# Kernel tuning notes

Hardware: AMD Instinct MI355X
Metric: run time of the kernel (lower is better)

## Reference

```python
import jax, jax.numpy as jnp
import numpy as np

BETA = 0.25
N_E = 8192
E_DIM = 256


def setup_inputs() -> dict:
    key = jax.random.key(0)
    k1, k2 = jax.random.split(key)
    z = jax.random.normal(k1, (16, E_DIM, 32, 32), dtype=jnp.float32)
    # matches torch init: uniform_(-1/n_e, 1/n_e)
    codebook = jax.random.uniform(k2, (N_E, E_DIM), dtype=jnp.float32,
                                  minval=-1.0 / N_E, maxval=1.0 / N_E)
    return {"z": z, "codebook": codebook}


def reference(z, codebook):
    B, C, H, W = z.shape  # C == e_dim
    zp = jnp.transpose(z, (0, 2, 3, 1))          # [B, H, W, C]
    zf = zp.reshape(-1, C)                       # [N, C], N = B*H*W
    # squared L2 distances: ||z||^2 + ||e||^2 - 2 z.e
    d = (jnp.sum(zf * zf, axis=1, keepdims=True)
         + jnp.sum(codebook * codebook, axis=1)
         - 2.0 * jnp.einsum('nc,kc->nk', zf, codebook))  # [N, n_e]
    min_encoding_indices = jnp.argmin(d, axis=1)         # [N]
    z_q = codebook[min_encoding_indices].reshape(zp.shape)  # [B, H, W, C]
    sg = jax.lax.stop_gradient
    loss = jnp.mean((sg(z_q) - zp) ** 2) + BETA * jnp.mean((z_q - sg(zp)) ** 2)
    # straight-through estimator
    z_q_st = zp + sg(z_q - zp)
    z_q_out = jnp.transpose(z_q_st, (0, 3, 1, 2))  # back to NCHW
    return z_q_out, loss, min_encoding_indices
```

## Files before the change

kernel.cpp:

```cpp
#include <hip/hip_runtime.h>

typedef short s8v __attribute__((ext_vector_type(8)));
typedef float f4v __attribute__((ext_vector_type(4)));
typedef float f4 __attribute__((ext_vector_type(4)));
typedef unsigned short u16v4 __attribute__((ext_vector_type(4)));

#define N_PIX 16384
#define NE    8192
#define EDIM  256
#define ZQ_ELEMS 4194304
#define MARGIN 4.5e-4f
#define NGRP 512

__device__ __forceinline__ float bf2f(unsigned short u) {
    union { unsigned int i; float f; } c; c.i = ((unsigned int)u) << 16; return c.f;
}
__device__ __forceinline__ unsigned short f2bf(float f) {
    unsigned int u = __float_as_uint(f);
    u = (u + 0x7fffu + ((u >> 16) & 1u)) >> 16;
    return (unsigned short)u;
}
__device__ __forceinline__ unsigned short f2bf_down(float f) {
    unsigned int u = __float_as_uint(f);
    unsigned short b = (unsigned short)(u >> 16);
    if ((u & 0xFFFFu) && (u >> 31)) b += 1;
    return b;
}

__device__ __forceinline__ float np_pw128sq(const float* a) {
    float r[8];
    #pragma unroll
    for (int j = 0; j < 8; ++j) r[j] = __fmul_rn(a[j], a[j]);
    for (int i = 8; i < 128; i += 8)
        #pragma unroll
        for (int j = 0; j < 8; ++j) r[j] = __fadd_rn(r[j], __fmul_rn(a[i + j], a[i + j]));
    return __fadd_rn(__fadd_rn(__fadd_rn(r[0], r[1]), __fadd_rn(r[2], r[3])),
                     __fadd_rn(__fadd_rn(r[4], r[5]), __fadd_rn(r[6], r[7])));
}


__global__ __launch_bounds__(256) void vq_pre(const float* __restrict__ z,
                                              const float* __restrict__ cb,
                                              unsigned short* __restrict__ z16,
                                              unsigned short* __restrict__ cb16,
                                              float* __restrict__ esum32,
                                              int do_z) {
    __shared__ unsigned short zl[64 * 66];
    int t = threadIdx.x;
    int bx = blockIdx.x;
    if (bx < 1024) {
        if (!do_z) return;
        int p0 = (bx >> 2) * 64;
        int c0 = (bx & 3) * 64;
        int b = p0 >> 10, hw0 = p0 & 1023;
        const float* src = z + (((size_t)b * 256 + c0) << 10) + hw0;
        #pragma unroll
        for (int i = 0; i < 4; ++i) {
            int idx = i * 256 + t;
            int ch = idx >> 4, pq = idx & 15;
            f4 v = *(const f4*)(src + ((size_t)ch << 10) + pq * 4);
            #pragma unroll
            for (int e = 0; e < 4; ++e) zl[(pq * 4 + e) * 66 + ch] = f2bf(v[e]);
        }
        __syncthreads();
        #pragma unroll
        for (int i = 0; i < 2; ++i) {
            int idx = i * 256 + t;
            int px = idx >> 3, cc = idx & 7;
            s8v o;
            #pragma unroll
            for (int e = 0; e < 8; ++e) o[e] = (short)zl[px * 66 + cc * 8 + e];
            *(s8v*)&z16[((size_t)(p0 + px)) * 256 + c0 + cc * 8] = o;
        }
    } else {
        int base = (bx - 1024) * 32;
        const float* src = cb + (size_t)base * EDIM;
        unsigned short* dst = cb16 + (size_t)base * EDIM;
        #pragma unroll
        for (int i = 0; i < 8; ++i) {
            int e0 = (i * 256 + t) * 4;
            f4 v = *(const f4*)(src + e0);
            u16v4 o;
            o.x = f2bf(v[0]); o.y = f2bf(v[1]); o.z = f2bf(v[2]); o.w = f2bf(v[3]);
            *(u16v4*)(dst + e0) = o;
        }
        if (t < 32) {
            const float* a = cb + (size_t)(base + t) * EDIM;
            esum32[base + t] = __fadd_rn(np_pw128sq(a), np_pw128sq(a + 128));
        }
    }
}

__global__ __launch_bounds__(512, 2) void vq_phase1g(const unsigned short* __restrict__ cb16,
                                                     const unsigned short* __restrict__ z16,
                                                     unsigned short* __restrict__ gmin) {
    __shared__ unsigned short L[2][32768];
    const int t = threadIdx.x;
    const int wave = t >> 6, lane = t & 63;
    const int q = lane >> 4, r = lane & 15;
    const int wr = wave >> 2, wc = wave & 3;
    const int cm0 = ((int)blockIdx.x >> 3) * 256;
    const int pg  = (int)blockIdx.x & 7;

    const int pc0 = t, pc1 = t + 512;
    const int row0 = pc0 >> 2, row1 = pc1 >> 2;
    const int lc0 = (pc0 & 3) ^ ((row0 >> 1) & 3);
    const int lc1 = (pc1 & 3) ^ ((row1 >> 1) & 3);
    const int go0 = row0 * 256 + lc0 * 8;
    const int go1 = row1 * 256 + lc1 * 8;
    const int ld0 = pc0 * 8;
    const int ld1 = pc1 * 8;

    const unsigned short* gA = cb16 + (size_t)cm0 * 256;
    const unsigned short* gB0 = z16 + (size_t)pg * 2048 * 256;

    f4v acc[8][4];
    const f4v zz = {0.f, 0.f, 0.f, 0.f};
    #pragma unroll
    for (int mi = 0; mi < 8; ++mi)
        #pragma unroll
        for (int ni = 0; ni < 4; ++ni) acc[mi][ni] = zz;

    const int cxo = (q ^ ((r >> 1) & 3)) * 8;
    const int aro = (wr * 128 + r) * 32 + cxo;
    const int bro = 16384 + (wc * 64 + r) * 32 + cxo;

#define GLL(g, l) __builtin_amdgcn_global_load_lds( \
        (const __attribute__((address_space(1))) unsigned int*)(g), \
        (__attribute__((address_space(3))) unsigned int*)(l), 16, 0, 0)
#define STAGEKT(buf_, gk_, gBp_) do { \
        unsigned short* Lb_ = &L[(buf_)][0]; \
        GLL(gA + go0 + (gk_),            Lb_ + ld0); \
        GLL(gA + go1 + (gk_),            Lb_ + ld1); \
        GLL(gA + go0 + 32 + (gk_),       Lb_ + 8192 + ld0); \
        GLL(gA + go1 + 32 + (gk_),       Lb_ + 8192 + ld1); \
        GLL((gBp_) + go0 + (gk_),        Lb_ + 16384 + ld0); \
        GLL((gBp_) + go1 + (gk_),        Lb_ + 16384 + ld1); \
        GLL((gBp_) + go0 + 32 + (gk_),   Lb_ + 16384 + 8192 + ld0); \
        GLL((gBp_) + go1 + 32 + (gk_),   Lb_ + 16384 + 8192 + ld1); } while (0)
#define ARD(Lp, mi, ks) (*(const s8v*)&(Lp)[(ks) * 8192 + (mi) * 512 + aro])
#define BRD(Lp, ni, ks) (*(const s8v*)&(Lp)[(ks) * 8192 + (ni) * 512 + bro])
#define MFMA16(Aset, Bset, mo) do { \
        __builtin_amdgcn_s_setprio(1); \
        _Pragma("unroll") \
        for (int mi = 0; mi < 4; ++mi) \
            _Pragma("unroll") \
            for (int ni = 0; ni < 4; ++ni) \
                acc[(mo) + mi][ni] = __builtin_amdgcn_mfma_f32_16x16x32_bf16( \
                    Aset[mi], Bset[ni], acc[(mo) + mi][ni], 0, 0, 0); \
        __builtin_amdgcn_s_setprio(0); } while (0)

    STAGEKT(0, 0, gB0);
    asm volatile("s_waitcnt vmcnt(0)" ::: "memory");
    __builtin_amdgcn_s_barrier();
    s8v A0[4], A1[4], B0[4], B1[4];
    #pragma unroll
    for (int ni = 0; ni < 4; ++ni) B0[ni] = BRD(&L[0][0], ni, 0);
    #pragma unroll
    for (int mi = 0; mi < 4; ++mi) A0[mi] = ARD(&L[0][0], mi, 0);

    for (int it = 0; it < 32; ++it) {
        const int buf = it & 1;
        const unsigned short* Lb = &L[buf][0];
        const unsigned short* Ln = &L[buf ^ 1][0];
        const int nit = it + 1;
        const bool st = nit < 32;

        __builtin_amdgcn_s_barrier();
        if (st) STAGEKT(buf ^ 1, (nit & 3) * 64, gB0 + (size_t)(nit >> 2) * 65536);

        #pragma unroll
        for (int mi = 0; mi < 4; ++mi) A1[mi] = ARD(Lb, 4 + mi, 0);
        __builtin_amdgcn_sched_barrier(0);
        MFMA16(A0, B0, 0);

        #pragma unroll
        for (int mi = 0; mi < 4; ++mi) A0[mi] = ARD(Lb, mi, 1);
        #pragma unroll
        for (int ni = 0; ni < 4; ++ni) B1[ni] = BRD(Lb, ni, 1);
        __builtin_amdgcn_sched_barrier(0);
        MFMA16(A1, B0, 4);

        #pragma unroll
        for (int mi = 0; mi < 4; ++mi) A1[mi] = ARD(Lb, 4 + mi, 1);
        __builtin_amdgcn_sched_barrier(0);
        MFMA16(A0, B1, 0);

        if (st) {
            asm volatile("s_waitcnt vmcnt(0)" ::: "memory");
            __builtin_amdgcn_s_barrier();
            #pragma unroll
            for (int ni = 0; ni < 4; ++ni) B0[ni] = BRD(Ln, ni, 0);
            #pragma unroll
            for (int mi = 0; mi < 4; ++mi) A0[mi] = ARD(Ln, mi, 0);
        }
        __builtin_amdgcn_sched_barrier(0);
        MFMA16(A1, B1, 4);

        if ((it & 3) == 3) {
            const int pn0 = pg * 2048 + (it >> 2) * 256;
            #pragma unroll
            for (int mi = 0; mi < 8; ++mi) {
                int g = cm0 / 16 + wr * 8 + mi;
                #pragma unroll
                for (int ni = 0; ni < 4; ++ni) {
                    f4v a = acc[mi][ni];
                    float mx = fmaxf(fmaxf(a[0], a[1]), fmaxf(a[2], a[3]));
                    mx = fmaxf(mx, __shfl_xor(mx, 16));
                    mx = fmaxf(mx, __shfl_xor(mx, 32));
                    if (q == 0) {
                        int pxc = (pn0 + wc * 64 + ni * 16) >> 4;
                        gmin[(size_t)pxc * 8192 + g * 16 + r] = f2bf_down(-2.0f * mx);
                    }
                    acc[mi][ni] = zz;
                }
            }
        }
    }
#undef MFMA16
#undef BRD
#undef ARD
#undef STAGEKT
#undef GLL
}

__global__ __launch_bounds__(512, 2) void vq_phase1(const float* __restrict__ z,
                                                    const unsigned short* __restrict__ cb16,
                                                    unsigned short* __restrict__ gmin) {
    const int t = threadIdx.x;
    const int wave = t >> 6, lane = t & 63;
    const int col = lane & 15, q = lane >> 4;
    const int mb = (blockIdx.x >> 1) * 64;
    const int chalf = blockIdx.x & 1;

    s8v Z[4][8];
    #pragma unroll
    for (int pt = 0; pt < 4; ++pt) {
        int n = mb + pt * 16 + col;
        const float* zb = z + ((size_t)(n >> 10) << 18) + (size_t)(n & 1023);
        #pragma unroll
        for (int c0 = 0; c0 < 8; ++c0) {
            s8v a;
            #pragma unroll
            for (int j = 0; j < 8; ++j) {
                int c = c0 * 32 + q * 8 + j;
                a[j] = (short)f2bf(zb[(size_t)c << 10]);
            }
            Z[pt][c0] = a;
        }
    }

    const int kbase = chalf * 4096 + wave * 512;
    for (int it = 0; it < 16; ++it) {
        int n0 = kbase + it * 32;
        const unsigned short* bb = cb16 + (size_t)(n0 + col) * EDIM + q * 8;
        f4v zz = {0.f, 0.f, 0.f, 0.f};
        f4v acc[4][2];
        #pragma unroll
        for (int pt = 0; pt < 4; ++pt) { acc[pt][0] = zz; acc[pt][1] = zz; }
        #pragma unroll
        for (int c0 = 0; c0 < 8; ++c0) {
            s8v C0 = *(const s8v*)(bb + c0 * 32);
            s8v C1 = *(const s8v*)(bb + 16 * EDIM + c0 * 32);
            #pragma unroll
            for (int pt = 0; pt < 4; ++pt) {
                acc[pt][0] = __builtin_amdgcn_mfma_f32_16x16x32_bf16(C0, Z[pt][c0], acc[pt][0], 0, 0, 0);
                acc[pt][1] = __builtin_amdgcn_mfma_f32_16x16x32_bf16(C1, Z[pt][c0], acc[pt][1], 0, 0, 0);
            }
        }
        int gbase = chalf * 256 + wave * 32 + it * 2;
        #pragma unroll
        for (int pt = 0; pt < 4; ++pt) {
            #pragma unroll
            for (int s = 0; s < 2; ++s) {
                f4v a = acc[pt][s];
                float mx = fmaxf(fmaxf(a[0], a[1]), fmaxf(a[2], a[3]));
                mx = fmaxf(mx, __shfl_xor(mx, 16));
                mx = fmaxf(mx, __shfl_xor(mx, 32));
                if (q == 0)
                    gmin[(size_t)((mb >> 4) + pt) * 8192 + (gbase + s) * 16 + col] =
                        f2bf_down(-2.0f * mx);
            }
        }
    }
}

__global__ __launch_bounds__(256) void vq_phase2(const float* __restrict__ z,
                                                 const float* __restrict__ cb,
                                                 const float* __restrict__ esum32,
                                                 const unsigned short* __restrict__ gmin,
                                                 unsigned int* __restrict__ idxw,
                                                 float* __restrict__ lossparts) {
    __shared__ float zt[32 * 260];
    __shared__ unsigned short gm[NGRP * 33];
    __shared__ float zs[32];
    __shared__ int pq;
    int t = threadIdx.x;
    int wave = t >> 6, lane = t & 63;
    int p0 = blockIdx.x * 32;
    int bb = p0 >> 10, inner = p0 & 1023;

    if (t == 0) pq = 0;
    const float* zb = z + (((size_t)bb * 256) << 10) + inner;
    #pragma unroll
    for (int i = 0; i < 8; ++i) {
        int job = i * 256 + t;
        int c = job >> 3, qq = job & 7;
        f4 v = *(const f4*)(zb + ((size_t)c << 10) + qq * 4);
        #pragma unroll
        for (int e = 0; e < 4; ++e) zt[(qq * 4 + e) * 260 + c] = v[e];
    }
    const unsigned short* gsrc = gmin + (size_t)(2 * blockIdx.x) * 8192;
    #pragma unroll
    for (int j = 0; j < 8; ++j) {
        int li8 = (j * 256 + t) * 8;
        s8v v = *(const s8v*)(gsrc + li8);
        int h = li8 >> 13, rem = li8 & 8191;
        int g = rem >> 4, r0 = rem & 15;
        #pragma unroll
        for (int e = 0; e < 8; ++e) gm[g * 33 + h * 16 + r0 + e] = (unsigned short)v[e];
    }
    __syncthreads();
    if (t < 32) {
        const float* a = zt + t * 260;
        zs[t] = __fadd_rn(np_pw128sq(a), np_pw128sq(a + 128));
    }
    __syncthreads();

#define DOT_TAIL(sv) do { sv += __shfl_xor(sv, 1); sv += __shfl_xor(sv, 2); } while (0)
#define MERGE(dv, kv) do { if ((dv) < bd || ((dv) == bd && (kv) < bk)) { bd = (dv); bk = (kv); } } while (0)

    float wls = 0.f;
    while (true) {
        int p;
        if (lane == 0) p = atomicAdd(&pq, 1);
        p = __shfl(p, 0);
        if (p >= 32) break;

        float lmin = 3.0e38f;
        #pragma unroll
        for (int j = 0; j < 8; ++j) lmin = fminf(lmin, bf2f(gm[(lane * 8 + j) * 33 + p]));
        #pragma unroll
        for (int m = 1; m < 64; m <<= 1) lmin = fminf(lmin, __shfl_xor(lmin, m));
        float thr = lmin + MARGIN;
        float zsp = zs[p];
        const f4* zr = (const f4*)(zt + p * 260) + (lane & 3);

        float bd = 3.0e38f; int bk = 0x7FFFFFFF;
        int pend = -1;
        for (int j = 0; j < 8; ++j) {
            unsigned long long mask = __ballot(bf2f(gm[(lane * 8 + j) * 33 + p]) <= thr);
            while (mask) {
                int lb = __builtin_ctzll(mask); mask &= mask - 1;
                int g = lb * 8 + j;
                if (pend < 0) { pend = g; continue; }
                int k1 = pend * 16 + (lane >> 2), k2 = g * 16 + (lane >> 2);
                const f4* c1 = (const f4*)(cb + (size_t)k1 * EDIM) + (lane & 3);
                const f4* c2 = (const f4*)(cb + (size_t)k2 * EDIM) + (lane & 3);
                double a0 = 0.0, a1 = 0.0, a2 = 0.0, a3 = 0.0;
                double b0 = 0.0, b1 = 0.0, b2 = 0.0, b3 = 0.0;
                #pragma unroll
                for (int i = 0; i < 16; ++i) {
                    f4 x = zr[i * 4], y1 = c1[i * 4], y2 = c2[i * 4];
                    a0 = fma((double)x[0], (double)y1[0], a0);
                    b0 = fma((double)x[0], (double)y2[0], b0);
                    a1 = fma((double)x[1], (double)y1[1], a1);
                    b1 = fma((double)x[1], (double)y2[1], b1);
                    a2 = fma((double)x[2], (double)y1[2], a2);
                    b2 = fma((double)x[2], (double)y2[2], b2);
                    a3 = fma((double)x[3], (double)y1[3], a3);
                    b3 = fma((double)x[3], (double)y2[3], b3);
                }
                double s1 = (a0 + a1) + (a2 + a3);
                double s2 = (b0 + b1) + (b2 + b3);
                DOT_TAIL(s1); DOT_TAIL(s2);
                float E1 = (float)s1, E2 = (float)s2;
                float d1 = __fsub_rn(__fadd_rn(zsp, esum32[k1]), __fmul_rn(2.0f, E1));
                float d2 = __fsub_rn(__fadd_rn(zsp, esum32[k2]), __fmul_rn(2.0f, E2));
                MERGE(d1, k1); MERGE(d2, k2);
                pend = -1;
            }
        }
        if (pend >= 0) {
            int k = pend * 16 + (lane >> 2);
            const f4* cr = (const f4*)(cb + (size_t)k * EDIM) + (lane & 3);
            double a0 = 0.0, a1 = 0.0, a2 = 0.0, a3 = 0.0;
            #pragma unroll
            for (int i = 0; i < 16; ++i) {
                f4 x = zr[i * 4], y = cr[i * 4];
                a0 = fma((double)x[0], (double)y[0], a0);
                a1 = fma((double)x[1], (double)y[1], a1);
                a2 = fma((double)x[2], (double)y[2], a2);
                a3 = fma((double)x[3], (double)y[3], a3);
            }
            double s = (a0 + a1) + (a2 + a3);
            DOT_TAIL(s);
            float E = (float)s;
            float d = __fsub_rn(__fadd_rn(zsp, esum32[k]), __fmul_rn(2.0f, E));
            MERGE(d, k);
        }
        #pragma unroll
        for (int m = 1; m < 64; m <<= 1) {
            float od = __shfl_xor(bd, m); int ok = __shfl_xor(bk, m);
            if (od < bd || (od == bd && ok < bk)) { bd = od; bk = ok; }
        }
        if (lane == 0) idxw[p0 + p] = (unsigned int)bk;

        float s0 = 0.f;
        #pragma unroll
        for (int e = 0; e < 4; ++e) {
            float cv = cb[(size_t)bk * EDIM + lane + 64 * e];
            float zv = zt[p * 260 + lane + 64 * e];
            float dx = cv - zv; s0 = fmaf(dx, dx, s0);
        }
        wls += s0;
    }
    #pragma unroll
    for (int m = 1; m < 64; m <<= 1) wls += __shfl_xor(wls, m);
    if (lane == 0)
        atomicAdd(&lossparts[(((int)blockIdx.x << 2) + wave) & 63], wls);
#undef MERGE
#undef DOT_TAIL
}

__global__ __launch_bounds__(256) void vq_emit(const float* __restrict__ cb,
                                               const unsigned int* __restrict__ idxw,
                                               const float* __restrict__ lossparts,
                                               float* __restrict__ outf) {
    __shared__ float qrow[1024 * 17];
    __shared__ unsigned int lidx[1024];
    int t = threadIdx.x;
    int gtid = blockIdx.x * 256 + t;
    if (gtid < N_PIX) outf[ZQ_ELEMS + 1 + gtid] = (float)(idxw[gtid] & (NE - 1));
    if (blockIdx.x == 0 && t < 64) {
        double v = (double)lossparts[t];
        #pragma unroll
        for (int m = 1; m < 64; m <<= 1) v += __shfl_xor(v, m);
        if (t == 0) outf[ZQ_ELEMS] = 1.25f * (float)(v * (1.0 / 4194304.0));
    }

    int b = blockIdx.x >> 4;
    int c0 = (blockIdx.x & 15) * 16;

    #pragma unroll
    for (int j = 0; j < 4; ++j)
        lidx[j * 256 + t] = idxw[b * 1024 + j * 256 + t] & (NE - 1);
    __syncthreads();
    #pragma unroll
    for (int j = 0; j < 16; ++j) {
        int p = j * 64 + (t >> 2);
        f4 v = *(const f4*)(cb + (size_t)lidx[p] * EDIM + c0 + (t & 3) * 4);
        #pragma unroll
        for (int e = 0; e < 4; ++e) qrow[p * 17 + (t & 3) * 4 + e] = v[e];
    }
    __syncthreads();

    size_t base = (size_t)blockIdx.x * 16384;
    #pragma unroll
    for (int i = 0; i < 16; ++i) {
        f4 v;
        #pragma unroll
        for (int e = 0; e < 4; ++e) v[e] = qrow[(t * 4 + e) * 17 + i];
        *(f4*)&outf[base + (size_t)i * 1024 + t * 4] = v;
    }
}

extern "C" void kernel_launch(void* const* d_in, const int* in_sizes, int n_in,
                              void* d_out, int out_size, void* d_ws, size_t ws_size,
                              hipStream_t stream) {
    const float* z  = (const float*)d_in[0];
    const float* cb = (const float*)d_in[1];
    float* outf = (float*)d_out;
    unsigned short* gmin = (unsigned short*)d_out;

    char* w = (char*)d_ws;
    unsigned short* cb16     = (unsigned short*)w;
    float*          esum32   = (float*)(w + 4194304);
    unsigned int*   idxw     = (unsigned int*)(w + 4227072);
    float*          lossparts= (float*)(w + 4292608);
    unsigned short* z16      = (unsigned short*)(w + 4292864);

    if (ws_size < 4292864) return;
    const bool big_ws = (ws_size >= 12681472);

    hipMemsetAsync(lossparts, 0, 256, stream);
    vq_pre<<<1280, 256, 0, stream>>>(z, cb, z16, cb16, esum32, big_ws ? 1 : 0);
    if (big_ws) {
        vq_phase1g<<<(NE / 256) * (N_PIX / 2048), 512, 0, stream>>>(cb16, z16, gmin);
    } else {
        vq_phase1 <<<(N_PIX / 64) * 2, 512, 0, stream>>>(z, cb16, gmin);
    }
    vq_phase2  <<<N_PIX / 32, 256, 0, stream>>>(z, cb, esum32, gmin, idxw, lossparts);
    vq_emit    <<<256, 256, 0, stream>>>(cb, idxw, lossparts, outf);
}
```

Baseline: 236.4 us.

## Halve K-tile and pixel chunk in GEMM kernel to raise occupancy and grid size

The codebook-by-pixel bf16 MFMA kernel now stages a 32-wide K slice per step instead of 64, halving LDS per block (64KB total) and raising launch bounds to 4 blocks per CU. Each block covers 1024 pixels instead of 2048, doubling the grid to 512 blocks. The software-pipelined register prefetch across iterations is replaced by a simpler load-then-compute loop, with a wait and barrier every step. The intent is more resident waves and better CU fill to hide latency, at the cost of more barriers per unit of work, less in-wave register pipelining, and possible register pressure under the tighter launch bound.

```diff
diff --git a/kernel.cpp b/kernel.cpp
--- a/kernel.cpp
+++ b/kernel.cpp
@@ -91,16 +91,16 @@
     }
 }
 
-__global__ __launch_bounds__(512, 2) void vq_phase1g(const unsigned short* __restrict__ cb16,
+__global__ __launch_bounds__(512, 4) void vq_phase1g(const unsigned short* __restrict__ cb16,
                                                      const unsigned short* __restrict__ z16,
                                                      unsigned short* __restrict__ gmin) {
-    __shared__ unsigned short L[2][32768];
+    __shared__ unsigned short L[2][16384];
     const int t = threadIdx.x;
     const int wave = t >> 6, lane = t & 63;
     const int q = lane >> 4, r = lane & 15;
     const int wr = wave >> 2, wc = wave & 3;
-    const int cm0 = ((int)blockIdx.x >> 3) * 256;
-    const int pg  = (int)blockIdx.x & 7;
+    const int cm0 = ((int)blockIdx.x >> 4) * 256;
+    const int pg  = (int)blockIdx.x & 15;
 
     const int pc0 = t, pc1 = t + 512;
     const int row0 = pc0 >> 2, row1 = pc1 >> 2;
@@ -112,7 +112,7 @@
     const int ld1 = pc1 * 8;
 
     const unsigned short* gA = cb16 + (size_t)cm0 * 256;
-    const unsigned short* gB0 = z16 + (size_t)pg * 2048 * 256;
+    const unsigned short* gB0 = z16 + (size_t)pg * 1024 * 256;
 
     f4v acc[8][4];
     const f4v zz = {0.f, 0.f, 0.f, 0.f};
@@ -123,82 +123,61 @@
 
     const int cxo = (q ^ ((r >> 1) & 3)) * 8;
     const int aro = (wr * 128 + r) * 32 + cxo;
-    const int bro = 16384 + (wc * 64 + r) * 32 + cxo;
+    const int bro = 8192 + (wc * 64 + r) * 32 + cxo;
 
 #define GLL(g, l) __builtin_amdgcn_global_load_lds( \
         (const __attribute__((address_space(1))) unsigned int*)(g), \
         (__attribute__((address_space(3))) unsigned int*)(l), 16, 0, 0)
 #define STAGEKT(buf_, gk_, gBp_) do { \
         unsigned short* Lb_ = &L[(buf_)][0]; \
-        GLL(gA + go0 + (gk_),            Lb_ + ld0); \
-        GLL(gA + go1 + (gk_),            Lb_ + ld1); \
-        GLL(gA + go0 + 32 + (gk_),       Lb_ + 8192 + ld0); \
-        GLL(gA + go1 + 32 + (gk_),       Lb_ + 8192 + ld1); \
-        GLL((gBp_) + go0 + (gk_),        Lb_ + 16384 + ld0); \
-        GLL((gBp_) + go1 + (gk_),        Lb_ + 16384 + ld1); \
-        GLL((gBp_) + go0 + 32 + (gk_),   Lb_ + 16384 + 8192 + ld0); \
-        GLL((gBp_) + go1 + 32 + (gk_),   Lb_ + 16384 + 8192 + ld1); } while (0)
-#define ARD(Lp, mi, ks) (*(const s8v*)&(Lp)[(ks) * 8192 + (mi) * 512 + aro])
-#define BRD(Lp, ni, ks) (*(const s8v*)&(Lp)[(ks) * 8192 + (ni) * 512 + bro])
-#define MFMA16(Aset, Bset, mo) do { \
-        __builtin_amdgcn_s_setprio(1); \
-        _Pragma("unroll") \
-        for (int mi = 0; mi < 4; ++mi) \
-            _Pragma("unroll") \
-            for (int ni = 0; ni < 4; ++ni) \
-                acc[(mo) + mi][ni] = __builtin_amdgcn_mfma_f32_16x16x32_bf16( \
-                    Aset[mi], Bset[ni], acc[(mo) + mi][ni], 0, 0, 0); \
-        __builtin_amdgcn_s_setprio(0); } while (0)
+        GLL(gA + go0 + (gk_),      Lb_ + ld0); \
+        GLL(gA + go1 + (gk_),      Lb_ + ld1); \
+        GLL((gBp_) + go0 + (gk_),  Lb_ + 8192 + ld0); \
+        GLL((gBp_) + go1 + (gk_),  Lb_ + 8192 + ld1); } while (0)
+#define ARD(Lp, mi) (*(const s8v*)&(Lp)[(mi) * 512 + aro])
+#define BRD(Lp, ni) (*(const s8v*)&(Lp)[(ni) * 512 + bro])
 
     STAGEKT(0, 0, gB0);
     asm volatile("s_waitcnt vmcnt(0)" ::: "memory");
     __builtin_amdgcn_s_barrier();
-    s8v A0[4], A1[4], B0[4], B1[4];
-    #pragma unroll
-    for (int ni = 0; ni < 4; ++ni) B0[ni] = BRD(&L[0][0], ni, 0);
-    #pragma unroll
-    for (int mi = 0; mi < 4; ++mi) A0[mi] = ARD(&L[0][0], mi, 0);
 
     for (int it = 0; it < 32; ++it) {
         const int buf = it & 1;
         const unsigned short* Lb = &L[buf][0];
-        const unsigned short* Ln = &L[buf ^ 1][0];
         const int nit = it + 1;
         const bool st = nit < 32;
 
+        if (st) STAGEKT(buf ^ 1, (nit & 7) * 32,
+                        gB0 + (size_t)(nit >> 3) * 65536);
+
+        s8v A0[4], A1[4], B0[4];
+        #pragma unroll
+        for (int ni = 0; ni < 4; ++ni) B0[ni] = BRD(Lb, ni);
+        #pragma unroll
+        for (int mi = 0; mi < 4; ++mi) A0[mi] = ARD(Lb, mi);
+        #pragma unroll
+        for (int mi = 0; mi < 4; ++mi) A1[mi] = ARD(Lb, 4 + mi);
+        __builtin_amdgcn_sched_barrier(0);
+        __builtin_amdgcn_s_setprio(1);
+        #pragma unroll
+        for (int mi = 0; mi < 4; ++mi)
+            #pragma unroll
+            for (int ni = 0; ni < 4; ++ni)
+                acc[mi][ni] = __builtin_amdgcn_mfma_f32_16x16x32_bf16(
+                    A0[mi], B0[ni], acc[mi][ni], 0, 0, 0);
+        #pragma unroll
+        for (int mi = 0; mi < 4; ++mi)
+            #pragma unroll
+            for (int ni = 0; ni < 4; ++ni)
+                acc[4 + mi][ni] = __builtin_amdgcn_mfma_f32_16x16x32_bf16(
+                    A1[mi], B0[ni], acc[4 + mi][ni], 0, 0, 0);
+        __builtin_amdgcn_s_setprio(0);
+
+        asm volatile("s_waitcnt vmcnt(0)" ::: "memory");
         __builtin_amdgcn_s_barrier();
-        if (st) STAGEKT(buf ^ 1, (nit & 3) * 64, gB0 + (size_t)(nit >> 2) * 65536);
-
-        #pragma unroll
-        for (int mi = 0; mi < 4; ++mi) A1[mi] = ARD(Lb, 4 + mi, 0);
-        __builtin_amdgcn_sched_barrier(0);
-        MFMA16(A0, B0, 0);
-
-        #pragma unroll
-        for (int mi = 0; mi < 4; ++mi) A0[mi] = ARD(Lb, mi, 1);
-        #pragma unroll
-        for (int ni = 0; ni < 4; ++ni) B1[ni] = BRD(Lb, ni, 1);
-        __builtin_amdgcn_sched_barrier(0);
-        MFMA16(A1, B0, 4);
-
-        #pragma unroll
-        for (int mi = 0; mi < 4; ++mi) A1[mi] = ARD(Lb, 4 + mi, 1);
-        __builtin_amdgcn_sched_barrier(0);
-        MFMA16(A0, B1, 0);
-
-        if (st) {
-            asm volatile("s_waitcnt vmcnt(0)" ::: "memory");
-            __builtin_amdgcn_s_barrier();
-            #pragma unroll
-            for (int ni = 0; ni < 4; ++ni) B0[ni] = BRD(Ln, ni, 0);
-            #pragma unroll
-            for (int mi = 0; mi < 4; ++mi) A0[mi] = ARD(Ln, mi, 0);
-        }
-        __builtin_amdgcn_sched_barrier(0);
-        MFMA16(A1, B1, 4);
-
-        if ((it & 3) == 3) {
-            const int pn0 = pg * 2048 + (it >> 2) * 256;
+
+        if ((it & 7) == 7) {
+            const int pn0 = pg * 1024 + (it >> 3) * 256;
             #pragma unroll
             for (int mi = 0; mi < 8; ++mi) {
                 int g = cm0 / 16 + wr * 8 + mi;
@@ -217,7 +196,6 @@
             }
         }
     }
-#undef MFMA16
 #undef BRD
 #undef ARD
 #undef STAGEKT
@@ -486,7 +464,7 @@
     hipMemsetAsync(lossparts, 0, 256, stream);
     vq_pre<<<1280, 256, 0, stream>>>(z, cb, z16, cb16, esum32, big_ws ? 1 : 0);
     if (big_ws) {
-        vq_phase1g<<<(NE / 256) * (N_PIX / 2048), 512, 0, stream>>>(cb16, z16, gmin);
+        vq_phase1g<<<(NE / 256) * (N_PIX / 1024), 512, 0, stream>>>(cb16, z16, gmin);
     } else {
         vq_phase1 <<<(N_PIX / 64) * 2, 512, 0, stream>>>(z, cb16, gmin);
     }
```

New measurement: 814.9 us. 3.45x slower.
